# Performance work log

Hardware: AMD Instinct MI355X
Metric: run time of the kernel (lower is better)

## Reference

```python
import jax, jax.numpy as jnp
import numpy as np

D_MODEL, D_STATE, D_CONV = 768, 8, 3
D_INNER = D_MODEL  # expand = 1
BATCH, SEQ = 4, 8192


def setup_inputs() -> dict:
    key = jax.random.key(0)
    ks = jax.random.split(key, 7)
    x = jax.random.normal(ks[0], (BATCH, SEQ, D_MODEL), dtype=jnp.float32)
    W_in = jax.random.normal(ks[1], (D_MODEL, 2 * D_INNER), dtype=jnp.float32) * 0.02
    conv_w = jax.random.normal(ks[2], (D_INNER, 1, D_CONV), dtype=jnp.float32) * 0.1
    conv_b = jnp.zeros((D_INNER,), dtype=jnp.float32)
    B = jax.random.normal(ks[3], (D_INNER, D_STATE), dtype=jnp.float32)
    C = jax.random.normal(ks[4], (D_INNER, D_STATE), dtype=jnp.float32)
    D = jnp.ones((D_INNER,), dtype=jnp.float32)
    W_out = jax.random.normal(ks[5], (D_INNER, D_MODEL), dtype=jnp.float32) * 0.02
    return {"x": x, "W_in": W_in, "conv_w": conv_w, "conv_b": conv_b,
            "B": B, "C": C, "D": D, "W_out": W_out}


def _forward(x, W_in, conv_w, conv_b, B, C, D, W_out):
    # in_proj and chunk
    xz = x @ W_in                                   # [B, L, 2*d_inner]
    xc, z = jnp.split(xz, 2, axis=-1)               # each [B, L, d_inner]
    # depthwise causal conv1d: torch pads (d_conv-1) both sides then slices [:L]
    # == left-pad (d_conv-1), no right pad
    xc = jnp.transpose(xc, (0, 2, 1))               # [B, d_inner, L]
    xc = jax.lax.conv_general_dilated(
        xc, conv_w,
        window_strides=(1,), padding=[(D_CONV - 1, 0)],
        dimension_numbers=("NCH", "OIH", "NCH"),
        feature_group_count=D_INNER)
    xc = xc + conv_b[None, :, None]
    xc = jnp.transpose(xc, (0, 2, 1))               # [B, L, d_inner]
    xc = jax.nn.silu(xc)
    z = jax.nn.silu(z)
    # simple SSM: h_t = h_{t-1} + outer(u_t, B); y_t = sum_s h_t*C + u_t*D
    # => y = cumsum_t(u) * sum_s(B*C) + u*D   (exact algebraic identity)
    BC = jnp.sum(B * C, axis=-1)                    # [d_inner]
    y = jnp.cumsum(xc, axis=1) * BC + xc * D
    out = (y * z) @ W_out                           # [B, L, d_model]
    return out


def reference(x, W_in, conv_w, conv_b, B, C, D, W_out):
    return _forward(x, W_in, conv_w, conv_b, B, C, D, W_out)
```

## Files before the change

### kernel.cpp

```cpp
#include <hip/hip_runtime.h>
#include <hip/hip_bf16.h>

#define D_MODEL 768
#define NSEQ    8192
#define NBATCH  4
#define MROWS   (NBATCH*NSEQ)
#define CHUNK   128
#define NCHUNK  (NSEQ/CHUNK)

#define BM 128
#define BN 192
#define BK 64

typedef __attribute__((ext_vector_type(8)))  short bshort8;
typedef __attribute__((ext_vector_type(16))) float f32x16;

__device__ __forceinline__ float bf2f(ushort u){
  union { unsigned int i; float f; } x; x.i = ((unsigned int)u) << 16; return x.f;
}
__device__ __forceinline__ ushort f2bf(float f){
  union { float f; unsigned int i; } x; x.f = f;
  unsigned int r = x.i + 0x7fffu + ((x.i >> 16) & 1u);
  return (ushort)(r >> 16);
}
__device__ __forceinline__ float silu_f(float v){ return v / (1.0f + __expf(-v)); }

__device__ __forceinline__ void async_copy16(const ushort* g, ushort* l){
  __builtin_amdgcn_global_load_lds((const __attribute__((address_space(1))) void*)g,
                                   (__attribute__((address_space(3))) void*)l, 16, 0, 0);
}

__global__ void tr_cvt(const float* __restrict__ in, ushort* __restrict__ out, int R, int C){
  __shared__ float tile[32][33];
  int c0 = blockIdx.x*32, r0 = blockIdx.y*32;
  int tx = threadIdx.x & 31, ty = threadIdx.x >> 5;
  #pragma unroll
  for (int p=0;p<4;p++){
    int r = ty + p*8;
    tile[r][tx] = in[(size_t)(r0+r)*C + c0 + tx];
  }
  __syncthreads();
  #pragma unroll
  for (int p=0;p<4;p++){
    int c = ty + p*8;
    out[(size_t)(c0+c)*R + r0 + tx] = f2bf(tile[tx][c]);
  }
}

__global__ void cvt_bf16(const float* __restrict__ in, ushort* __restrict__ out, int n){
  int i = (blockIdx.x*256 + threadIdx.x)*8;
  if (i >= n) return;
  const float4 f0 = *(const float4*)(in + i);
  const float4 f1 = *(const float4*)(in + i + 4);
  ushort o[8];
  o[0]=f2bf(f0.x); o[1]=f2bf(f0.y); o[2]=f2bf(f0.z); o[3]=f2bf(f0.w);
  o[4]=f2bf(f1.x); o[5]=f2bf(f1.y); o[6]=f2bf(f1.z); o[7]=f2bf(f1.w);
  *(ulonglong2*)(out + i) = *(const ulonglong2*)o;
}

__global__ __launch_bounds__(256) void gemm1_bt(
    const ushort* __restrict__ A, const ushort* __restrict__ BT,
    ushort* __restrict__ oxc, ushort* __restrict__ oz, int K)
{
  __shared__ __align__(16) ushort Asm[BM*BK];
  __shared__ __align__(16) ushort Bsm[BN*BK];
  const int tid = threadIdx.x;
  const int bm = blockIdx.x, bn = blockIdx.y;
  const int lane = tid & 63, wid = tid >> 6;
  const int wm = (wid >> 1) * 64, wn = (wid & 1) * 96;
  const int l31 = lane & 31, half = lane >> 5;

  const ushort* Ag[4]; ushort* Al[4];
  #pragma unroll
  for (int it=0; it<4; ++it){
    int p  = it*256 + tid;
    int r  = p >> 3;
    int cl = (p & 7) ^ (r & 7);
    Ag[it] = A + (size_t)(bm*BM + r)*K + cl*8;
    Al[it] = Asm + p*8;
  }
  const ushort* Bg[6]; ushort* Bl[6];
  #pragma unroll
  for (int it=0; it<6; ++it){
    int p  = it*256 + tid;
    int r  = p >> 3;
    int cl = (p & 7) ^ (r & 7);
    Bg[it] = BT + (size_t)(bn*BN + r)*K + cl*8;
    Bl[it] = Bsm + p*8;
  }

  int arow[2], ar7[2], brow[3], br7[3];
  #pragma unroll
  for (int i=0;i<2;i++){
    int ra = wm + i*32 + l31; arow[i] = ra*BK; ar7[i] = ra & 7;
  }
  #pragma unroll
  for (int j=0;j<3;j++){
    int rb = wn + j*32 + l31; brow[j] = rb*BK; br7[j] = rb & 7;
  }

  f32x16 acc[2][3];
  #pragma unroll
  for (int i=0;i<2;i++)
    #pragma unroll
    for (int j=0;j<3;j++)
      #pragma unroll
      for (int r=0;r<16;r++) acc[i][j][r] = 0.f;

  const int KT = K / BK;
  for (int kt=0; kt<KT; ++kt){
    __syncthreads();
    #pragma unroll
    for (int it=0; it<4; ++it){ async_copy16(Ag[it], Al[it]); Ag[it] += BK; }
    #pragma unroll
    for (int it=0; it<6; ++it){ async_copy16(Bg[it], Bl[it]); Bg[it] += BK; }
    asm volatile("s_waitcnt vmcnt(0)" ::: "memory");
    __syncthreads();

    #pragma unroll
    for (int s=0; s<4; ++s){
      const int c = s*2 + half;
      bshort8 av[2], bv[3];
      #pragma unroll
      for (int i=0;i<2;i++)
        av[i] = *(const bshort8*)(Asm + arow[i] + ((c ^ ar7[i]) << 3));
      #pragma unroll
      for (int j=0;j<3;j++)
        bv[j] = *(const bshort8*)(Bsm + brow[j] + ((c ^ br7[j]) << 3));
      #pragma unroll
      for (int i=0;i<2;i++)
        #pragma unroll
        for (int j=0;j<3;j++)
          acc[i][j] = __builtin_amdgcn_mfma_f32_32x32x16_bf16(av[i], bv[j], acc[i][j], 0,0,0);
    }
  }

  if (bn < 4){
    #pragma unroll
    for (int i=0;i<2;i++){
      const int Rbase = bm*BM + wm + i*32 + 4*half;
      #pragma unroll
      for (int j=0;j<3;j++){
        const int Cc = bn*BN + wn + j*32 + l31;
        #pragma unroll
        for (int reg=0; reg<16; reg++){
          const int R = Rbase + (reg & 3) + 8*(reg >> 2);
          oxc[(size_t)R*768 + Cc] = f2bf(acc[i][j][reg]);
        }
      }
    }
  } else {
    #pragma unroll
    for (int i=0;i<2;i++){
      const int Rbase = bm*BM + wm + i*32 + 4*half;
      #pragma unroll
      for (int j=0;j<3;j++){
        const int Cc = bn*BN - 768 + wn + j*32 + l31;
        #pragma unroll
        for (int reg=0; reg<16; reg++){
          const int R = Rbase + (reg & 3) + 8*(reg >> 2);
          oz[(size_t)R*768 + Cc] = f2bf(silu_f(acc[i][j][reg]));
        }
      }
    }
  }
}

#define BM2 64
__global__ __launch_bounds__(256) void gemm2_bt(
    const ushort* __restrict__ A, const ushort* __restrict__ BT,
    float* __restrict__ of, int K)
{
  __shared__ __align__(16) ushort Asm[BM2*BK];
  __shared__ __align__(16) ushort Bsm[BN*BK];
  const int tid = threadIdx.x;
  const int bm = blockIdx.x, bn = blockIdx.y;
  const int lane = tid & 63, wid = tid >> 6;
  const int wm = (wid >> 1) * 32, wn = (wid & 1) * 96;
  const int l31 = lane & 31, half = lane >> 5;

  const ushort* Ag[2]; ushort* Al[2];
  #pragma unroll
  for (int it=0; it<2; ++it){
    int p  = it*256 + tid;
    int r  = p >> 3;
    int cl = (p & 7) ^ (r & 7);
    Ag[it] = A + (size_t)(bm*BM2 + r)*K + cl*8;
    Al[it] = Asm + p*8;
  }
  const ushort* Bg[6]; ushort* Bl[6];
  #pragma unroll
  for (int it=0; it<6; ++it){
    int p  = it*256 + tid;
    int r  = p >> 3;
    int cl = (p & 7) ^ (r & 7);
    Bg[it] = BT + (size_t)(bn*BN + r)*K + cl*8;
    Bl[it] = Bsm + p*8;
  }

  int arow, ar7, brow[3], br7[3];
  { int ra = wm + l31; arow = ra*BK; ar7 = ra & 7; }
  #pragma unroll
  for (int j=0;j<3;j++){
    int rb = wn + j*32 + l31; brow[j] = rb*BK; br7[j] = rb & 7;
  }

  f32x16 acc[3];
  #pragma unroll
  for (int j=0;j<3;j++)
    #pragma unroll
    for (int r=0;r<16;r++) acc[j][r] = 0.f;

  const int KT = K / BK;
  for (int kt=0; kt<KT; ++kt){
    __syncthreads();
    #pragma unroll
    for (int it=0; it<2; ++it){ async_copy16(Ag[it], Al[it]); Ag[it] += BK; }
    #pragma unroll
    for (int it=0; it<6; ++it){ async_copy16(Bg[it], Bl[it]); Bg[it] += BK; }
    asm volatile("s_waitcnt vmcnt(0)" ::: "memory");
    __syncthreads();

    #pragma unroll
    for (int s=0; s<4; ++s){
      const int c = s*2 + half;
      bshort8 av, bv[3];
      av = *(const bshort8*)(Asm + arow + ((c ^ ar7) << 3));
      #pragma unroll
      for (int j=0;j<3;j++)
        bv[j] = *(const bshort8*)(Bsm + brow[j] + ((c ^ br7[j]) << 3));
      #pragma unroll
      for (int j=0;j<3;j++)
        acc[j] = __builtin_amdgcn_mfma_f32_32x32x16_bf16(av, bv[j], acc[j], 0,0,0);
    }
  }

  const int Rbase = bm*BM2 + wm + 4*half;
  #pragma unroll
  for (int j=0;j<3;j++){
    const int Cc = bn*BN + wn + j*32 + l31;
    #pragma unroll
    for (int reg=0; reg<16; reg++){
      const int R = Rbase + (reg & 3) + 8*(reg >> 2);
      of[(size_t)R*768 + Cc] = acc[j][reg];
    }
  }
}

__global__ void conv_psum(const ushort* __restrict__ xc, const float* __restrict__ cw,
                          const float* __restrict__ cb, float* __restrict__ psum){
  int c0 = threadIdx.x * 2;
  int b = blockIdx.z, ch = blockIdx.x;
  int t0 = ch*CHUNK;
  const ushort* xp = xc + (size_t)b*NSEQ*768 + c0;
  float w0a=cw[c0*3+0], w1a=cw[c0*3+1], w2a=cw[c0*3+2], ba=cb[c0];
  float w0b=cw[c0*3+3], w1b=cw[c0*3+4], w2b=cw[c0*3+5], bb=cb[c0+1];
  float am2=0.f, am1=0.f, bm2=0.f, bm1=0.f;
  if (t0>=2){ ushort2 u = *(const ushort2*)(xp + (size_t)(t0-2)*768); am2=bf2f(u.x); bm2=bf2f(u.y); }
  if (t0>=1){ ushort2 u = *(const ushort2*)(xp + (size_t)(t0-1)*768); am1=bf2f(u.x); bm1=bf2f(u.y); }
  float sa=0.f, sb=0.f;
  #pragma unroll 4
  for (int i=0;i<CHUNK;i++){
    ushort2 u = *(const ushort2*)(xp + (size_t)(t0+i)*768);
    float xa = bf2f(u.x), xb = bf2f(u.y);
    sa += silu_f(w0a*am2 + w1a*am1 + w2a*xa + ba);
    sb += silu_f(w0b*bm2 + w1b*bm1 + w2b*xb + bb);
    am2=am1; am1=xa; bm2=bm1; bm1=xb;
  }
  float2* pp = (float2*)(psum + ((size_t)b*NCHUNK + ch)*768 + c0);
  *pp = make_float2(sa, sb);
}

__global__ void scan_chunks(const float* __restrict__ psum, float* __restrict__ offs){
  int idx = blockIdx.x*256 + threadIdx.x;
  int b = idx/768, c = idx%768;
  float run = 0.f;
  for (int ch=0; ch<NCHUNK; ch++){
    size_t o = ((size_t)b*NCHUNK + ch)*768 + c;
    offs[o] = run;
    run += psum[o];
  }
}

__global__ void scan_apply(const ushort* __restrict__ xc, const ushort* __restrict__ zb,
                           const float* __restrict__ cw, const float* __restrict__ cb,
                           const float* __restrict__ Bm, const float* __restrict__ Cm,
                           const float* __restrict__ Dv, const float* __restrict__ offs,
                           ushort* __restrict__ v){
  int c0 = threadIdx.x * 2;
  int b = blockIdx.z, ch = blockIdx.x;
  int t0 = ch*CHUNK;
  size_t base = (size_t)b*NSEQ*768 + c0;
  const ushort* xp = xc + base;
  const ushort* zp = zb + base;
  ushort* vp = v + base;
  float w0a=cw[c0*3+0], w1a=cw[c0*3+1], w2a=cw[c0*3+2], ba=cb[c0];
  float w0b=cw[c0*3+3], w1b=cw[c0*3+4], w2b=cw[c0*3+5], bb=cb[c0+1];
  float bca=0.f, bcb=0.f;
  #pragma unroll
  for (int s=0;s<8;s++){ bca += Bm[c0*8+s]*Cm[c0*8+s]; bcb += Bm[c0*8+8+s]*Cm[c0*8+8+s]; }
  float dda = Dv[c0], ddb = Dv[c0+1];
  const float2 off2 = *(const float2*)(offs + ((size_t)b*NCHUNK + ch)*768 + c0);
  float cua = off2.x, cub = off2.y;
  float am2=0.f, am1=0.f, bm2=0.f, bm1=0.f;
  if (t0>=2){ ushort2 u = *(const ushort2*)(xp + (size_t)(t0-2)*768); am2=bf2f(u.x); bm2=bf2f(u.y); }
  if (t0>=1){ ushort2 u = *(const ushort2*)(xp + (size_t)(t0-1)*768); am1=bf2f(u.x); bm1=bf2f(u.y); }
  #pragma unroll 4
  for (int i=0;i<CHUNK;i++){
    size_t o = (size_t)(t0+i)*768;
    ushort2 u = *(const ushort2*)(xp + o);
    ushort2 z2 = *(const ushort2*)(zp + o);
    float xa = bf2f(u.x), xb = bf2f(u.y);
    float ua = silu_f(w0a*am2 + w1a*am1 + w2a*xa + ba);
    float ub = silu_f(w0b*bm2 + w1b*bm1 + w2b*xb + bb);
    cua += ua; cub += ub;
    float ya = bca*cua + dda*ua;
    float yb = bcb*cub + ddb*ub;
    ushort2 o2; o2.x = f2bf(ya * bf2f(z2.x)); o2.y = f2bf(yb * bf2f(z2.y));
    *(ushort2*)(vp + o) = o2;
    am2=am1; am1=xa; bm2=bm1; bm1=xb;
  }
}

extern "C" void kernel_launch(void* const* d_in, const int* in_sizes, int n_in,
                              void* d_out, int out_size, void* d_ws, size_t ws_size,
                              hipStream_t stream)
{
  const float* x      = (const float*)d_in[0];
  const float* W_in   = (const float*)d_in[1];
  const float* conv_w = (const float*)d_in[2];
  const float* conv_b = (const float*)d_in[3];
  const float* Bm     = (const float*)d_in[4];
  const float* Cm     = (const float*)d_in[5];
  const float* Dv     = (const float*)d_in[6];
  const float* W_out  = (const float*)d_in[7];
  float* out = (float*)d_out;

  char* ws = (char*)d_ws;
  ushort* xbf   = (ushort*)(ws + 0);
  ushort* xcbf  = (ushort*)(ws + 50331648);
  ushort* zbf   = (ushort*)(ws + 100663296);
  ushort* wint  = (ushort*)(ws + 150994944);
  ushort* woutt = (ushort*)(ws + 153354240);
  float*  psum  = (float*)(ws + 154533888);
  float*  offs  = (float*)(ws + 155320320);
  if (ws_size < 156106752) return;

  tr_cvt<<<dim3(1536/32, 768/32), 256, 0, stream>>>(W_in,  wint,  768, 1536);
  tr_cvt<<<dim3(768/32,  768/32), 256, 0, stream>>>(W_out, woutt, 768, 768);
  cvt_bf16<<<(MROWS*768)/2048, 256, 0, stream>>>(x, xbf, MROWS*768);

  gemm1_bt<<<dim3(MROWS/BM, 1536/BN), 256, 0, stream>>>(xbf, wint, xcbf, zbf, 768);

  conv_psum  <<<dim3(NCHUNK, 1, NBATCH), 384, 0, stream>>>(xcbf, conv_w, conv_b, psum);
  scan_chunks<<<12, 256, 0, stream>>>(psum, offs);
  scan_apply <<<dim3(NCHUNK, 1, NBATCH), 384, 0, stream>>>(xcbf, zbf, conv_w, conv_b,
                                                           Bm, Cm, Dv, offs, xbf );

  gemm2_bt<<<dim3(MROWS/BM2, 768/BN), 256, 0, stream>>>(xbf, woutt, out, 768);
}
```

Baseline: 412.6 us.

## Double-buffer LDS tiles in both GEMM kernels to overlap loads with MFMA

Both GEMM kernels now keep two shared-memory buffers for the A and B tiles. The first tile is prefetched before the loop, and each later iteration issues the async global-to-LDS copies for the next K tile while the MFMAs run on the current one. This removes one barrier per iteration and is meant to hide global memory latency behind compute. In exchange, LDS use per block doubles, which can lower the number of blocks resident per CU.

Result: slower. 430.0 us (+4.2%).

```diff
diff --git a/kernel.cpp b/kernel.cpp
--- a/kernel.cpp
+++ b/kernel.cpp
@@ -62,31 +62,31 @@
     const ushort* __restrict__ A, const ushort* __restrict__ BT,
     ushort* __restrict__ oxc, ushort* __restrict__ oz, int K)
 {
-  __shared__ __align__(16) ushort Asm[BM*BK];
-  __shared__ __align__(16) ushort Bsm[BN*BK];
+  __shared__ __align__(16) ushort Asm[2][BM*BK];
+  __shared__ __align__(16) ushort Bsm[2][BN*BK];
   const int tid = threadIdx.x;
   const int bm = blockIdx.x, bn = blockIdx.y;
   const int lane = tid & 63, wid = tid >> 6;
   const int wm = (wid >> 1) * 64, wn = (wid & 1) * 96;
   const int l31 = lane & 31, half = lane >> 5;
 
-  const ushort* Ag[4]; ushort* Al[4];
+  const ushort* Ag[4]; int aoff[4];
   #pragma unroll
   for (int it=0; it<4; ++it){
     int p  = it*256 + tid;
     int r  = p >> 3;
     int cl = (p & 7) ^ (r & 7);
     Ag[it] = A + (size_t)(bm*BM + r)*K + cl*8;
-    Al[it] = Asm + p*8;
-  }
-  const ushort* Bg[6]; ushort* Bl[6];
+    aoff[it] = p*8;
+  }
+  const ushort* Bg[6]; int boff[6];
   #pragma unroll
   for (int it=0; it<6; ++it){
     int p  = it*256 + tid;
     int r  = p >> 3;
     int cl = (p & 7) ^ (r & 7);
     Bg[it] = BT + (size_t)(bn*BN + r)*K + cl*8;
-    Bl[it] = Bsm + p*8;
+    boff[it] = p*8;
   }
 
   int arow[2], ar7[2], brow[3], br7[3];
@@ -108,31 +108,43 @@
       for (int r=0;r<16;r++) acc[i][j][r] = 0.f;
 
   const int KT = K / BK;
+
+  #pragma unroll
+  for (int it=0; it<4; ++it){ async_copy16(Ag[it], &Asm[0][aoff[it]]); Ag[it] += BK; }
+  #pragma unroll
+  for (int it=0; it<6; ++it){ async_copy16(Bg[it], &Bsm[0][boff[it]]); Bg[it] += BK; }
+
+  int cur = 0;
   for (int kt=0; kt<KT; ++kt){
-    __syncthreads();
-    #pragma unroll
-    for (int it=0; it<4; ++it){ async_copy16(Ag[it], Al[it]); Ag[it] += BK; }
-    #pragma unroll
-    for (int it=0; it<6; ++it){ async_copy16(Bg[it], Bl[it]); Bg[it] += BK; }
+    __builtin_amdgcn_sched_barrier(0);
     asm volatile("s_waitcnt vmcnt(0)" ::: "memory");
-    __syncthreads();
-
+    __builtin_amdgcn_s_barrier();
+    __builtin_amdgcn_sched_barrier(0);
+    if (kt+1 < KT){
+      #pragma unroll
+      for (int it=0; it<4; ++it){ async_copy16(Ag[it], &Asm[cur^1][aoff[it]]); Ag[it] += BK; }
+      #pragma unroll
+      for (int it=0; it<6; ++it){ async_copy16(Bg[it], &Bsm[cur^1][boff[it]]); Bg[it] += BK; }
+    }
+    const ushort* As = &Asm[cur][0];
+    const ushort* Bs = &Bsm[cur][0];
     #pragma unroll
     for (int s=0; s<4; ++s){
       const int c = s*2 + half;
       bshort8 av[2], bv[3];
       #pragma unroll
       for (int i=0;i<2;i++)
-        av[i] = *(const bshort8*)(Asm + arow[i] + ((c ^ ar7[i]) << 3));
+        av[i] = *(const bshort8*)(As + arow[i] + ((c ^ ar7[i]) << 3));
       #pragma unroll
       for (int j=0;j<3;j++)
-        bv[j] = *(const bshort8*)(Bsm + brow[j] + ((c ^ br7[j]) << 3));
+        bv[j] = *(const bshort8*)(Bs + brow[j] + ((c ^ br7[j]) << 3));
       #pragma unroll
       for (int i=0;i<2;i++)
         #pragma unroll
         for (int j=0;j<3;j++)
           acc[i][j] = __builtin_amdgcn_mfma_f32_32x32x16_bf16(av[i], bv[j], acc[i][j], 0,0,0);
     }
+    cur ^= 1;
   }
 
   if (bn < 4){
@@ -171,31 +183,31 @@
     const ushort* __restrict__ A, const ushort* __restrict__ BT,
     float* __restrict__ of, int K)
 {
-  __shared__ __align__(16) ushort Asm[BM2*BK];
-  __shared__ __align__(16) ushort Bsm[BN*BK];
+  __shared__ __align__(16) ushort Asm[2][BM2*BK];
+  __shared__ __align__(16) ushort Bsm[2][BN*BK];
   const int tid = threadIdx.x;
   const int bm = blockIdx.x, bn = blockIdx.y;
   const int lane = tid & 63, wid = tid >> 6;
   const int wm = (wid >> 1) * 32, wn = (wid & 1) * 96;
   const int l31 = lane & 31, half = lane >> 5;
 
-  const ushort* Ag[2]; ushort* Al[2];
+  const ushort* Ag[2]; int aoff[2];
   #pragma unroll
   for (int it=0; it<2; ++it){
     int p  = it*256 + tid;
     int r  = p >> 3;
     int cl = (p & 7) ^ (r & 7);
     Ag[it] = A + (size_t)(bm*BM2 + r)*K + cl*8;
-    Al[it] = Asm + p*8;
-  }
-  const ushort* Bg[6]; ushort* Bl[6];
+    aoff[it] = p*8;
+  }
+  const ushort* Bg[6]; int boff[6];
   #pragma unroll
   for (int it=0; it<6; ++it){
     int p  = it*256 + tid;
     int r  = p >> 3;
     int cl = (p & 7) ^ (r & 7);
     Bg[it] = BT + (size_t)(bn*BN + r)*K + cl*8;
-    Bl[it] = Bsm + p*8;
+    boff[it] = p*8;
   }
 
   int arow, ar7, brow[3], br7[3];
@@ -212,27 +224,39 @@
     for (int r=0;r<16;r++) acc[j][r] = 0.f;
 
   const int KT = K / BK;
+
+  #pragma unroll
+  for (int it=0; it<2; ++it){ async_copy16(Ag[it], &Asm[0][aoff[it]]); Ag[it] += BK; }
+  #pragma unroll
+  for (int it=0; it<6; ++it){ async_copy16(Bg[it], &Bsm[0][boff[it]]); Bg[it] += BK; }
+
+  int cur = 0;
   for (int kt=0; kt<KT; ++kt){
-    __syncthreads();
-    #pragma unroll
-    for (int it=0; it<2; ++it){ async_copy16(Ag[it], Al[it]); Ag[it] += BK; }
-    #pragma unroll
-    for (int it=0; it<6; ++it){ async_copy16(Bg[it], Bl[it]); Bg[it] += BK; }
+    __builtin_amdgcn_sched_barrier(0);
     asm volatile("s_waitcnt vmcnt(0)" ::: "memory");
-    __syncthreads();
-
+    __builtin_amdgcn_s_barrier();
+    __builtin_amdgcn_sched_barrier(0);
+    if (kt+1 < KT){
+      #pragma unroll
+      for (int it=0; it<2; ++it){ async_copy16(Ag[it], &Asm[cur^1][aoff[it]]); Ag[it] += BK; }
+      #pragma unroll
+      for (int it=0; it<6; ++it){ async_copy16(Bg[it], &Bsm[cur^1][boff[it]]); Bg[it] += BK; }
+    }
+    const ushort* As = &Asm[cur][0];
+    const ushort* Bs = &Bsm[cur][0];
     #pragma unroll
     for (int s=0; s<4; ++s){
       const int c = s*2 + half;
       bshort8 av, bv[3];
-      av = *(const bshort8*)(Asm + arow + ((c ^ ar7) << 3));
+      av = *(const bshort8*)(As + arow + ((c ^ ar7) << 3));
       #pragma unroll
       for (int j=0;j<3;j++)
-        bv[j] = *(const bshort8*)(Bsm + brow[j] + ((c ^ br7[j]) << 3));
+        bv[j] = *(const bshort8*)(Bs + brow[j] + ((c ^ br7[j]) << 3));
       #pragma unroll
       for (int j=0;j<3;j++)
         acc[j] = __builtin_amdgcn_mfma_f32_32x32x16_bf16(av, bv[j], acc[j], 0,0,0);
     }
+    cur ^= 1;
   }
 
   const int Rbase = bm*BM2 + wm + 4*half;
```
